# Optimization experiments

Measured on AMD Instinct MI355X. Metric: run time of the kernel, lower is better.

## Reference

```python
import jax, jax.numpy as jnp
import numpy as np

B, LATENT, LOCAL, HIDDEN, H, W = 512, 256, 256, 512, 16, 16


def setup_inputs() -> dict:
    key = jax.random.key(0)
    ks = jax.random.split(key, 7)
    anchor = jax.random.normal(ks[0], (B, LATENT), dtype=jnp.float32)
    positive = jax.random.normal(ks[1], (B, LOCAL, H, W), dtype=jnp.float32)
    # MLP params (Linear: y = x @ W + b), scaled like Kaiming-uniform-ish init
    W1 = jax.random.normal(ks[2], (LATENT, HIDDEN), dtype=jnp.float32) / np.sqrt(LATENT)
    b1 = jnp.zeros((HIDDEN,), dtype=jnp.float32)
    W2 = jax.random.normal(ks[3], (HIDDEN, LATENT), dtype=jnp.float32) / np.sqrt(HIDDEN)
    b2 = jnp.zeros((LATENT,), dtype=jnp.float32)
    # self.W: Linear(latent -> local, bias=False)
    Wc = jax.random.normal(ks[4], (LATENT, LOCAL), dtype=jnp.float32) / np.sqrt(LATENT)
    return {"anchor": anchor, "positive": positive, "W1": W1, "b1": b1,
            "W2": W2, "b2": b2, "Wc": Wc}


def reference(anchor, positive, W1, b1, W2, b2, Wc):
    # residual MLP on anchor: anchor + MLP(anchor)
    a = anchor + (jax.nn.relu(anchor @ W1 + b1) @ W2 + b2)  # [b, latent]
    pred = a @ Wc                                            # [b, local]
    b, c, h, w = positive.shape
    pos = positive.reshape(b, c, h * w)                      # [b, c, hw]
    # fused batched matmul over all h*w locations:
    # logits[k, i, j] = sum_c pred[i, c] * positive[j, c, k]
    logits = jnp.einsum('ic,jck->kij', pred, pos)            # [hw, b, b]
    # row-wise max subtraction (over the contrast dim, dim=1 in torch)
    logits = logits - jnp.max(logits, axis=2, keepdims=True)
    return logits  # stacked version of the torch list of h*w [b, b] matrices
```

## Files before the change

kernel.cpp:

```cpp
#include <hip/hip_runtime.h>
#include <hip/hip_bf16.h>

typedef unsigned short u16;
typedef unsigned int u32;
typedef __attribute__((ext_vector_type(8))) short short8;
typedef __attribute__((ext_vector_type(4))) float f32x4;

#define B_   512
#define C_   256
#define HID_ 512
#define HW_  256

__device__ __forceinline__ u16 f2b(float f) {
    union { float f; u32 i; } v; v.f = f;
    u32 x = v.i;
    u32 r = (x + 0x7fffu + ((x >> 16) & 1u)) >> 16;
    return (u16)r;
}
__device__ __forceinline__ float b2f(u16 u) {
    union { u32 i; float f; } v; v.i = ((u32)u) << 16; return v.f;
}

__global__ __launch_bounds__(256) void k_mlp(
        const float* __restrict__ anchor, const float* __restrict__ W1,
        const float* __restrict__ b1, const float* __restrict__ W2,
        const float* __restrict__ b2, const float* __restrict__ Wc,
        u16* __restrict__ pred)
{
    const int row0 = blockIdx.x * 4, t = threadIdx.x;
    __shared__ float a_sh[4][C_];
    __shared__ float h_sh[4][HID_];
    __shared__ float a2_sh[4][C_];

    #pragma unroll
    for (int r = 0; r < 4; ++r) a_sh[r][t] = anchor[(size_t)(row0 + r) * C_ + t];
    __syncthreads();

    float h0[4], h1[4];
    {
        float2 bb = *(const float2*)&b1[2 * t];
        #pragma unroll
        for (int r = 0; r < 4; ++r) { h0[r] = bb.x; h1[r] = bb.y; }
    }
    for (int l = 0; l < C_; ++l) {
        float2 w = *(const float2*)&W1[(size_t)l * HID_ + 2 * t];
        #pragma unroll
        for (int r = 0; r < 4; ++r) {
            float a = a_sh[r][l];
            h0[r] += a * w.x;
            h1[r] += a * w.y;
        }
    }
    #pragma unroll
    for (int r = 0; r < 4; ++r) {
        h_sh[r][2 * t]     = fmaxf(h0[r], 0.f);
        h_sh[r][2 * t + 1] = fmaxf(h1[r], 0.f);
    }
    __syncthreads();

    float a2[4];
    {
        float bv = b2[t];
        #pragma unroll
        for (int r = 0; r < 4; ++r) a2[r] = a_sh[r][t] + bv;
    }
    for (int h = 0; h < HID_; ++h) {
        float w = W2[(size_t)h * C_ + t];
        #pragma unroll
        for (int r = 0; r < 4; ++r) a2[r] += h_sh[r][h] * w;
    }
    #pragma unroll
    for (int r = 0; r < 4; ++r) a2_sh[r][t] = a2[r];
    __syncthreads();

    float p[4] = {0.f, 0.f, 0.f, 0.f};
    for (int d = 0; d < C_; ++d) {
        float w = Wc[(size_t)d * C_ + t];
        #pragma unroll
        for (int r = 0; r < 4; ++r) p[r] += a2_sh[r][d] * w;
    }
    #pragma unroll
    for (int r = 0; r < 4; ++r) pred[(size_t)(row0 + r) * C_ + t] = f2b(p[r]);
}

__global__ __launch_bounds__(512) void k_einsum(
        const float* __restrict__ positive, const u16* __restrict__ pred,
        u16* __restrict__ ws2)
{
    const int bx = blockIdx.x;
    const int kt = bx & 1;
    const int j  = bx >> 1;
    const int k0 = kt * 128;

    const int tid  = threadIdx.x;
    const int lane = tid & 63, w = tid >> 6;
    const int q = lane >> 4, m = lane & 15;
    const int wk = w & 1, wi = w >> 1;

    __shared__ uint4 At[128 * 16];

    const float* pos_j = positive + (size_t)j * (C_ * HW_);

    f32x4 acc[4][8];
    #pragma unroll
    for (int a = 0; a < 4; ++a)
        #pragma unroll
        for (int b = 0; b < 8; ++b) acc[a][b] = f32x4{0.f, 0.f, 0.f, 0.f};

    const int co = tid >> 5, ko = tid & 31;

    for (int c0 = 0; c0 < C_; c0 += 128) {
        {
            u32 pk[4][4];
            const float* base = pos_j + (size_t)(c0 + co * 8) * HW_ + k0 + ko;
            #pragma unroll
            for (int cr = 0; cr < 8; ++cr) {
                #pragma unroll
                for (int kkk = 0; kkk < 4; ++kkk) {
                    u16 b = f2b(base[(size_t)cr * HW_ + kkk * 32]);
                    if ((cr & 1) == 0) pk[kkk][cr >> 1] = (u32)b;
                    else               pk[kkk][cr >> 1] |= ((u32)b) << 16;
                }
            }
            #pragma unroll
            for (int kkk = 0; kkk < 4; ++kkk) {
                const int kl = ko + kkk * 32;
                uint4 o; o.x = pk[kkk][0]; o.y = pk[kkk][1];
                o.z = pk[kkk][2]; o.w = pk[kkk][3];
                At[kl * 16 + (co ^ (kl & 15))] = o;
            }
        }
        __syncthreads();

        #pragma unroll
        for (int s = 0; s < 4; ++s) {
            union { uint4 u; short8 v; } af[4], bf;
            #pragma unroll
            for (int mt = 0; mt < 4; ++mt) {
                const int kl = wk * 64 + mt * 16 + m;
                af[mt].u = At[kl * 16 + ((s * 4 + q) ^ (kl & 15))];
            }
            #pragma unroll
            for (int nt = 0; nt < 8; ++nt) {
                const int i_ = wi * 128 + nt * 16 + m;
                bf.u = *(const uint4*)&pred[(size_t)i_ * C_ + c0 + s * 32 + q * 8];
                #pragma unroll
                for (int mt = 0; mt < 4; ++mt)
                    acc[mt][nt] = __builtin_amdgcn_mfma_f32_16x16x32_bf16(
                        af[mt].v, bf.v, acc[mt][nt], 0, 0, 0);
            }
        }
        __syncthreads();
    }

    #pragma unroll
    for (int mt = 0; mt < 4; ++mt) {
        #pragma unroll
        for (int nt = 0; nt < 8; ++nt) {
            const int i_ = wi * 128 + nt * 16 + m;
            #pragma unroll
            for (int r = 0; r < 4; ++r) {
                const int k_ = k0 + wk * 64 + mt * 16 + q * 4 + r;
                ws2[((size_t)j * HW_ + k_) * B_ + i_] = f2b(acc[mt][nt][r]);
            }
        }
    }
}

__global__ __launch_bounds__(256) void k_maxsub(
        const u16* __restrict__ ws2, float* __restrict__ out)
{
    const int bx = blockIdx.x;
    const int k  = bx >> 3;
    const int i0 = (bx & 7) * 64;
    const int t  = threadIdx.x;

    __shared__ u16 tile[512 * 66];
    __shared__ float maxp[4][64];
    __shared__ float maxv[64];

    {
        const int jr = t >> 5, lane5 = t & 31;
        for (int p = 0; p < 64; ++p) {
            const int jj = p * 8 + jr;
            u32 v = *(const u32*)&ws2[((size_t)jj * HW_ + k) * B_ + i0 + lane5 * 2];
            *(u32*)&tile[jj * 66 + lane5 * 2] = v;
        }
    }
    __syncthreads();

    {
        const int i = t & 63, jq = t >> 6;
        float pm = -3.4e38f;
        for (int r = 0; r < 128; ++r) {
            const int jj = jq * 128 + r;
            pm = fmaxf(pm, b2f(tile[jj * 66 + i]));
        }
        maxp[jq][i] = pm;
    }
    __syncthreads();
    if (t < 64)
        maxv[t] = fmaxf(fmaxf(maxp[0][t], maxp[1][t]),
                        fmaxf(maxp[2][t], maxp[3][t]));
    __syncthreads();

    {
        const int ir = t >> 5, jr = t & 31;
        #pragma unroll
        for (int p = 0; p < 8; ++p) {
            const int i_loc = p * 8 + ir;
            const float mv = maxv[i_loc];
            float* orow = out + ((size_t)k * B_ + i0 + i_loc) * B_;
            #pragma unroll
            for (int c = 0; c < 16; ++c) {
                const int jj = c * 32 + jr;
                orow[jj] = b2f(tile[jj * 66 + i_loc]) - mv;
            }
        }
    }
}

extern "C" void kernel_launch(void* const* d_in, const int* in_sizes, int n_in,
                              void* d_out, int out_size, void* d_ws, size_t ws_size,
                              hipStream_t stream)
{
    const float* anchor   = (const float*)d_in[0];
    const float* positive = (const float*)d_in[1];
    const float* W1 = (const float*)d_in[2];
    const float* b1 = (const float*)d_in[3];
    const float* W2 = (const float*)d_in[4];
    const float* b2 = (const float*)d_in[5];
    const float* Wc = (const float*)d_in[6];
    float* out = (float*)d_out;

    u16* pred = (u16*)d_ws;
    u16* ws2  = (u16*)((char*)d_ws + (size_t)B_ * C_ * 2);

    k_mlp<<<B_ / 4, 256, 0, stream>>>(anchor, W1, b1, W2, b2, Wc, pred);
    k_einsum<<<B_ * 2, 512, 0, stream>>>(positive, pred, ws2);
    k_maxsub<<<HW_ * 8, 256, 0, stream>>>(ws2, out);
}
```

Measured before the change: 563.4 us.

## Transpose positive to bf16 layout, fuse per-location GEMM with row-max subtraction

Adds a transpose kernel that converts positive to bf16 in a [hw, b, c] layout. A new GEMM kernel then computes each location's full 512-wide logits row block with MFMA, staging operands into LDS via global_load_lds DMA. The row max and subtraction happen in registers before float output is written. This removes the bf16 intermediate round-trip and the separate max-subtract kernel, at the cost of an extra transposed copy of positive in workspace. It also drops the bf16 rounding of logits before the max.

```diff
diff --git a/kernel.cpp b/kernel.cpp
--- a/kernel.cpp
+++ b/kernel.cpp
@@ -21,6 +21,12 @@
     union { u32 i; float f; } v; v.i = ((u32)u) << 16; return v.f;
 }
 
+__device__ __forceinline__ void dma16(const u16* g, u16* l) {
+    __builtin_amdgcn_global_load_lds(
+        (const __attribute__((address_space(1))) u32*)g,
+        (__attribute__((address_space(3))) u32*)l, 16, 0, 0);
+}
+
 __global__ __launch_bounds__(256) void k_mlp(
         const float* __restrict__ anchor, const float* __restrict__ W1,
         const float* __restrict__ b1, const float* __restrict__ W2,
@@ -83,23 +89,66 @@
     for (int r = 0; r < 4; ++r) pred[(size_t)(row0 + r) * C_ + t] = f2b(p[r]);
 }
 
-__global__ __launch_bounds__(512) void k_einsum(
-        const float* __restrict__ positive, const u16* __restrict__ pred,
-        u16* __restrict__ ws2)
+__global__ __launch_bounds__(256) void k_transpose(
+        const float* __restrict__ positive, u16* __restrict__ P)
 {
     const int bx = blockIdx.x;
-    const int kt = bx & 1;
-    const int j  = bx >> 1;
-    const int k0 = kt * 128;
+    const int j  = bx >> 2;
+    const int k0 = (bx & 3) * 64;
+    const int t  = threadIdx.x;
+
+    __shared__ float Tf[64][68];
+
+    const float* pj = positive + (size_t)j * (C_ * HW_);
+
+    for (int p = 0; p < 4; ++p) {
+        const int c0 = p * 64;
+        {
+            const int kk = t & 15, cr = t >> 4;
+            #pragma unroll
+            for (int s = 0; s < 4; ++s) {
+                const int cl = s * 16 + cr;
+                float4 v = *(const float4*)&pj[(size_t)(c0 + cl) * HW_ + k0 + kk * 4];
+                *(float4*)&Tf[cl][kk * 4] = v;
+            }
+        }
+        __syncthreads();
+        {
+            const int kr = t >> 2, cq = t & 3;
+            u32 wpk[8];
+            #pragma unroll
+            for (int y = 0; y < 16; y += 2) {
+                u16 lo = f2b(Tf[cq * 16 + y][kr]);
+                u16 hi = f2b(Tf[cq * 16 + y + 1][kr]);
+                wpk[y >> 1] = (u32)lo | ((u32)hi << 16);
+            }
+            u16* dst = P + ((size_t)(k0 + kr) * B_ + j) * C_ + c0 + cq * 16;
+            ((uint4*)dst)[0] = make_uint4(wpk[0], wpk[1], wpk[2], wpk[3]);
+            ((uint4*)dst)[1] = make_uint4(wpk[4], wpk[5], wpk[6], wpk[7]);
+        }
+        __syncthreads();
+    }
+}
+
+__global__ __launch_bounds__(512, 2) void k_gemm_fused(
+        const u16* __restrict__ P, const u16* __restrict__ pred,
+        float* __restrict__ out)
+{
+    const int bx = blockIdx.x;
+    const int k  = bx >> 2;
+    const int i0 = (bx & 3) * 128;
+
+    __shared__ u16 Bsm[B_ * 32];
+    __shared__ u16 Asm[128 * 32];
+    __shared__ float maxw[128][4];
+    __shared__ float maxv[128];
 
     const int tid  = threadIdx.x;
     const int lane = tid & 63, w = tid >> 6;
     const int q = lane >> 4, m = lane & 15;
-    const int wk = w & 1, wi = w >> 1;
-
-    __shared__ uint4 At[128 * 16];
-
-    const float* pos_j = positive + (size_t)j * (C_ * HW_);
+    const int wi = w >> 2, wj = w & 3;
+
+    const u16* Pk = P + (size_t)k * (B_ * C_);
 
     f32x4 acc[4][8];
     #pragma unroll
@@ -107,115 +156,81 @@
         #pragma unroll
         for (int b = 0; b < 8; ++b) acc[a][b] = f32x4{0.f, 0.f, 0.f, 0.f};
 
-    const int co = tid >> 5, ko = tid & 31;
-
-    for (int c0 = 0; c0 < C_; c0 += 128) {
+    for (int ch = 0; ch < 8; ++ch) {
+        const int c0 = ch * 32;
+        __syncthreads();
+        #pragma unroll
+        for (int r = 0; r < 4; ++r) {
+            const int jb  = w * 64 + r * 16 + (lane >> 2);
+            const int oct = lane & 3;
+            dma16(Pk + (size_t)jb * C_ + c0 + oct * 8,
+                  Bsm + (size_t)(w * 256 + r * 64) * 8);
+        }
         {
-            u32 pk[4][4];
-            const float* base = pos_j + (size_t)(c0 + co * 8) * HW_ + k0 + ko;
-            #pragma unroll
-            for (int cr = 0; cr < 8; ++cr) {
-                #pragma unroll
-                for (int kkk = 0; kkk < 4; ++kkk) {
-                    u16 b = f2b(base[(size_t)cr * HW_ + kkk * 32]);
-                    if ((cr & 1) == 0) pk[kkk][cr >> 1] = (u32)b;
-                    else               pk[kkk][cr >> 1] |= ((u32)b) << 16;
-                }
-            }
-            #pragma unroll
-            for (int kkk = 0; kkk < 4; ++kkk) {
-                const int kl = ko + kkk * 32;
-                uint4 o; o.x = pk[kkk][0]; o.y = pk[kkk][1];
-                o.z = pk[kkk][2]; o.w = pk[kkk][3];
-                At[kl * 16 + (co ^ (kl & 15))] = o;
-            }
-        }
-        __syncthreads();
-
-        #pragma unroll
-        for (int s = 0; s < 4; ++s) {
-            union { uint4 u; short8 v; } af[4], bf;
-            #pragma unroll
-            for (int mt = 0; mt < 4; ++mt) {
-                const int kl = wk * 64 + mt * 16 + m;
-                af[mt].u = At[kl * 16 + ((s * 4 + q) ^ (kl & 15))];
-            }
-            #pragma unroll
-            for (int nt = 0; nt < 8; ++nt) {
-                const int i_ = wi * 128 + nt * 16 + m;
-                bf.u = *(const uint4*)&pred[(size_t)i_ * C_ + c0 + s * 32 + q * 8];
-                #pragma unroll
-                for (int mt = 0; mt < 4; ++mt)
-                    acc[mt][nt] = __builtin_amdgcn_mfma_f32_16x16x32_bf16(
-                        af[mt].v, bf.v, acc[mt][nt], 0, 0, 0);
-            }
-        }
-        __syncthreads();
-    }
+            const int ia  = w * 16 + (lane >> 2);
+            const int oct = lane & 3;
+            dma16(pred + (size_t)(i0 + ia) * C_ + c0 + oct * 8,
+                  Asm + (size_t)(w * 64) * 8);
+        }
+        __syncthreads();
+
+        union { uint4 u; short8 v; } af[4], bf[8];
+        #pragma unroll
+        for (int mt = 0; mt < 4; ++mt)
+            af[mt].u = *(const uint4*)&Asm[((wi * 64 + mt * 16 + m) * 4 + q) * 8];
+        #pragma unroll
+        for (int nt = 0; nt < 8; ++nt)
+            bf[nt].u = *(const uint4*)&Bsm[((wj * 128 + nt * 16 + m) * 4 + q) * 8];
+        #pragma unroll
+        for (int mt = 0; mt < 4; ++mt)
+            #pragma unroll
+            for (int nt = 0; nt < 8; ++nt)
+                acc[mt][nt] = __builtin_amdgcn_mfma_f32_16x16x32_bf16(
+                    af[mt].v, bf[nt].v, acc[mt][nt], 0, 0, 0);
+    }
+
+    float pm[4][4];
+    #pragma unroll
+    for (int mt = 0; mt < 4; ++mt)
+        #pragma unroll
+        for (int r = 0; r < 4; ++r) {
+            float v = acc[mt][0][r];
+            #pragma unroll
+            for (int nt = 1; nt < 8; ++nt) v = fmaxf(v, acc[mt][nt][r]);
+            pm[mt][r] = v;
+        }
+    #pragma unroll
+    for (int d = 1; d < 16; d <<= 1) {
+        #pragma unroll
+        for (int mt = 0; mt < 4; ++mt)
+            #pragma unroll
+            for (int r = 0; r < 4; ++r)
+                pm[mt][r] = fmaxf(pm[mt][r], __shfl_xor(pm[mt][r], d, 64));
+    }
+    __syncthreads();
+    if (m == 0) {
+        #pragma unroll
+        for (int mt = 0; mt < 4; ++mt)
+            #pragma unroll
+            for (int r = 0; r < 4; ++r)
+                maxw[wi * 64 + mt * 16 + q * 4 + r][wj] = pm[mt][r];
+    }
+    __syncthreads();
+    if (tid < 128)
+        maxv[tid] = fmaxf(fmaxf(maxw[tid][0], maxw[tid][1]),
+                          fmaxf(maxw[tid][2], maxw[tid][3]));
+    __syncthreads();
 
     #pragma unroll
     for (int mt = 0; mt < 4; ++mt) {
         #pragma unroll
-        for (int nt = 0; nt < 8; ++nt) {
-            const int i_ = wi * 128 + nt * 16 + m;
-            #pragma unroll
-            for (int r = 0; r < 4; ++r) {
-                const int k_ = k0 + wk * 64 + mt * 16 + q * 4 + r;
-                ws2[((size_t)j * HW_ + k_) * B_ + i_] = f2b(acc[mt][nt][r]);
-            }
-        }
-    }
-}
-
-__global__ __launch_bounds__(256) void k_maxsub(
-        const u16* __restrict__ ws2, float* __restrict__ out)
-{
-    const int bx = blockIdx.x;
-    const int k  = bx >> 3;
-    const int i0 = (bx & 7) * 64;
-    const int t  = threadIdx.x;
-
-    __shared__ u16 tile[512 * 66];
-    __shared__ float maxp[4][64];
-    __shared__ float maxv[64];
-
-    {
-        const int jr = t >> 5, lane5 = t & 31;
-        for (int p = 0; p < 64; ++p) {
-            const int jj = p * 8 + jr;
-            u32 v = *(const u32*)&ws2[((size_t)jj * HW_ + k) * B_ + i0 + lane5 * 2];
-            *(u32*)&tile[jj * 66 + lane5 * 2] = v;
-        }
-    }
-    __syncthreads();
-
-    {
-        const int i = t & 63, jq = t >> 6;
-        float pm = -3.4e38f;
-        for (int r = 0; r < 128; ++r) {
-            const int jj = jq * 128 + r;
-            pm = fmaxf(pm, b2f(tile[jj * 66 + i]));
-        }
-        maxp[jq][i] = pm;
-    }
-    __syncthreads();
-    if (t < 64)
-        maxv[t] = fmaxf(fmaxf(maxp[0][t], maxp[1][t]),
-                        fmaxf(maxp[2][t], maxp[3][t]));
-    __syncthreads();
-
-    {
-        const int ir = t >> 5, jr = t & 31;
-        #pragma unroll
-        for (int p = 0; p < 8; ++p) {
-            const int i_loc = p * 8 + ir;
-            const float mv = maxv[i_loc];
-            float* orow = out + ((size_t)k * B_ + i0 + i_loc) * B_;
-            #pragma unroll
-            for (int c = 0; c < 16; ++c) {
-                const int jj = c * 32 + jr;
-                orow[jj] = b2f(tile[jj * 66 + i_loc]) - mv;
-            }
+        for (int r = 0; r < 4; ++r) {
+            const int i_ = i0 + wi * 64 + mt * 16 + q * 4 + r;
+            const float mv = maxv[wi * 64 + mt * 16 + q * 4 + r];
+            float* orow = out + ((size_t)k * B_ + i_) * B_ + wj * 128;
+            #pragma unroll
+            for (int nt = 0; nt < 8; ++nt)
+                orow[nt * 16 + m] = acc[mt][nt][r] - mv;
         }
     }
 }
@@ -234,9 +249,9 @@
     float* out = (float*)d_out;
 
     u16* pred = (u16*)d_ws;
-    u16* ws2  = (u16*)((char*)d_ws + (size_t)B_ * C_ * 2);
+    u16* P    = (u16*)((char*)d_ws + (size_t)B_ * C_ * 2);
 
     k_mlp<<<B_ / 4, 256, 0, stream>>>(anchor, W1, b1, W2, b2, Wc, pred);
-    k_einsum<<<B_ * 2, 512, 0, stream>>>(positive, pred, ws2);
-    k_maxsub<<<HW_ * 8, 256, 0, stream>>>(ws2, out);
-}
+    k_transpose<<<B_ * 4, 256, 0, stream>>>(positive, P);
+    k_gemm_fused<<<HW_ * 4, 512, 0, stream>>>(P, pred, out);
+}
```

Measured after the change: 505.7 us. 1.11x faster.
